# Kernel tuning notes

Hardware: AMD Instinct MI355X
Metric: run time of the kernel (lower is better)

Reference implementation:

```python
import jax, jax.numpy as jnp
import numpy as np
import math

D_MODEL = 1024
N_HEADS = 16
HEAD_DIM = D_MODEL // N_HEADS
N_LEVELS = 4
B = 8
MAX_LEN = 1024
LN_EPS = 1e-5


def setup_inputs() -> dict:
    key = jax.random.key(0)
    ks = jax.random.split(key, 6)
    lengths = np.array([1024, 768, 512, 896, 640, 1024, 576, 704], dtype=np.int32)
    N = int(lengths.sum())  # 6144
    batch_offsets = jnp.asarray(np.concatenate([[0], np.cumsum(lengths)]).astype(np.int32))
    x = jax.random.normal(ks[0], (N, D_MODEL), jnp.float32)
    levels = jax.random.randint(ks[1], (N, 1), 0, N_LEVELS).astype(jnp.float32)
    coords = jax.random.uniform(ks[2], (N, 2), jnp.float32) * 64.0
    positions = jnp.concatenate([levels, coords], axis=-1)  # [N, 3] = (level, y, x)
    ln_gamma = jnp.ones((D_MODEL,), jnp.float32)
    ln_beta = jnp.zeros((D_MODEL,), jnp.float32)
    w_qkv = jax.random.normal(ks[3], (D_MODEL, 3 * D_MODEL), jnp.float32) / math.sqrt(D_MODEL)
    w_out = jax.random.normal(ks[4], (D_MODEL, D_MODEL), jnp.float32) / math.sqrt(D_MODEL)
    # learned per-level, per-head rotary frequencies for 2 spatial coords
    base = 10.0 ** (-2.0 * np.arange(HEAD_DIM // 2) / HEAD_DIM)  # rope_theta = 10.0
    rope_freqs = (jnp.asarray(base, jnp.float32)[None, None, :, None]
                  * (1.0 + 0.1 * jax.random.normal(ks[5], (N_LEVELS, N_HEADS, HEAD_DIM // 2, 2), jnp.float32)))
    return {"x": x, "positions": positions, "batch_offsets": batch_offsets,
            "ln_gamma": ln_gamma, "ln_beta": ln_beta, "w_qkv": w_qkv,
            "w_out": w_out, "rope_freqs": rope_freqs}


def _layernorm(x, g, b):
    mu = jnp.mean(x, axis=-1, keepdims=True)
    var = jnp.mean(jnp.square(x - mu), axis=-1, keepdims=True)
    return (x - mu) * jax.lax.rsqrt(var + LN_EPS) * g + b


def _forward(x, positions, batch_offsets, ln_gamma, ln_beta, w_qkv, w_out, rope_freqs):
    N = x.shape[0]
    residual = x
    h = _layernorm(x, ln_gamma, ln_beta)
    q, k, v = jnp.split(h @ w_qkv, 3, axis=-1)  # each [N, D]

    # ragged -> padded batch layout
    tok = jnp.arange(N)
    batch_ids = jnp.searchsorted(batch_offsets[1:], tok, side='right')  # [N]
    pos_in_seq = tok - batch_offsets[batch_ids]                         # [N]
    lengths = batch_offsets[1:] - batch_offsets[:-1]                    # [B]
    valid = jnp.arange(MAX_LEN)[None, :] < lengths[:, None]             # [B, L]

    def pad(t, fill=0.0):
        out = jnp.full((B, MAX_LEN) + t.shape[1:], fill, t.dtype)
        return out.at[batch_ids, pos_in_seq].set(t)

    qp = pad(q).reshape(B, MAX_LEN, N_HEADS, HEAD_DIM)
    kp = pad(k).reshape(B, MAX_LEN, N_HEADS, HEAD_DIM)
    vp = pad(v).reshape(B, MAX_LEN, N_HEADS, HEAD_DIM)
    posp = pad(positions, fill=1.0)  # padded positions filled with ones (as in torch code)

    # multilevel RoPE: per-level learned freqs over 2 spatial coords
    lvl = jnp.clip(posp[..., 0].astype(jnp.int32), 0, N_LEVELS - 1)  # [B, L]
    f = rope_freqs[lvl]                                              # [B, L, H, K, 2]
    ang = jnp.einsum('blhkc,blc->blhk', f, posp[..., 1:])            # [B, L, H, K]
    cos, sin = jnp.cos(ang), jnp.sin(ang)

    def rot(t):  # rotate consecutive pairs of head_dim
        t = t.reshape(B, MAX_LEN, N_HEADS, HEAD_DIM // 2, 2)
        a, b = t[..., 0], t[..., 1]
        return jnp.stack([a * cos - b * sin, a * sin + b * cos], axis=-1).reshape(
            B, MAX_LEN, N_HEADS, HEAD_DIM)

    qr, kr = rot(qp), rot(kp)

    # masked SDPA (padded keys excluded; padded query rows are dropped on un-pad)
    scale = 1.0 / math.sqrt(HEAD_DIM)
    scores = jnp.einsum('blhd,bmhd->bhlm', qr, kr) * scale
    scores = jnp.where(valid[:, None, None, :], scores, jnp.float32(-1e9))
    attn = jax.nn.softmax(scores, axis=-1)
    o = jnp.einsum('bhlm,bmhd->blhd', attn, vp).reshape(B, MAX_LEN, D_MODEL)

    o = o[batch_ids, pos_in_seq]  # back to packed [N, D]
    return o @ w_out + residual


def reference(x, positions, batch_offsets, ln_gamma, ln_beta, w_qkv, w_out, rope_freqs):
    return _forward(x, positions, batch_offsets, ln_gamma, ln_beta, w_qkv, w_out, rope_freqs)
```

## Files before the change

### kernel.cpp

```cpp
#include <hip/hip_runtime.h>


typedef float  f32x4  __attribute__((ext_vector_type(4)));
typedef __bf16 bf16x8 __attribute__((ext_vector_type(8)));
typedef __bf16 bf16x4 __attribute__((ext_vector_type(4)));
typedef short  s16x4  __attribute__((ext_vector_type(4)));
typedef short  s16x8  __attribute__((ext_vector_type(8)));
typedef unsigned short u16x4 __attribute__((ext_vector_type(4)));

typedef __attribute__((address_space(1))) void as1_void_t;
typedef __attribute__((address_space(3))) void as3_void_t;

static __device__ __forceinline__ unsigned short f2bf(float f) {
  unsigned int u = __float_as_uint(f);
  u += 0x7fffu + ((u >> 16) & 1u);
  return (unsigned short)(u >> 16);
}
static __device__ __forceinline__ float bf2f(unsigned short s) {
  return __uint_as_float(((unsigned int)s) << 16);
}

static __device__ __forceinline__ void gload_lds16(const void* g, void* l) {
  __builtin_amdgcn_global_load_lds((as1_void_t*)g, (as3_void_t*)l, 16, 0, 0);
}

static __device__ __forceinline__ f32x4 mfma32(bf16x8 a, bf16x8 b, f32x4 c) {
  return __builtin_amdgcn_mfma_f32_16x16x32_bf16(a, b, c, 0, 0, 0);
}
static __device__ __forceinline__ f32x4 mfma16(s16x4 a, s16x4 b, f32x4 c) {
  return __builtin_amdgcn_mfma_f32_16x16x16bf16_1k(a, b, c, 0, 0, 0);
}

__global__ __launch_bounds__(256) void ln_kernel(
    const float* __restrict__ x, const float* __restrict__ gamma,
    const float* __restrict__ beta, unsigned short* __restrict__ h, int Ntok) {
  int row  = blockIdx.x * 4 + (threadIdx.x >> 6);
  int lane = threadIdx.x & 63;
  const float* xr = x + (size_t)row * 1024;
  f32x4 v[4];
  float s = 0.f, ss = 0.f;
#pragma unroll
  for (int c = 0; c < 4; ++c) {
    v[c] = *(const f32x4*)(xr + c * 256 + lane * 4);
#pragma unroll
    for (int j = 0; j < 4; ++j) { s += v[c][j]; ss += v[c][j] * v[c][j]; }
  }
#pragma unroll
  for (int d = 1; d < 64; d <<= 1) {
    s  += __shfl_xor(s, d);
    ss += __shfl_xor(ss, d);
  }
  float mu  = s * (1.f / 1024.f);
  float var = ss * (1.f / 1024.f) - mu * mu;
  float inv = rsqrtf(var + 1e-5f);
#pragma unroll
  for (int c = 0; c < 4; ++c) {
    f32x4 gv = *(const f32x4*)(gamma + c * 256 + lane * 4);
    f32x4 bv = *(const f32x4*)(beta  + c * 256 + lane * 4);
    u16x4 hv;
#pragma unroll
    for (int j = 0; j < 4; ++j) hv[j] = f2bf((v[c][j] - mu) * inv * gv[j] + bv[j]);
    *(u16x4*)(h + (size_t)row * 1024 + c * 256 + lane * 4) = hv;
  }
}

__global__ __launch_bounds__(256) void transpose_bf16(
    const float* __restrict__ in, unsigned short* __restrict__ out, int R, int C) {
  __shared__ unsigned short tile[64][65];
  int c0 = blockIdx.x * 64, r0 = blockIdx.y * 64;
  int t = threadIdx.x;
  int tr = t >> 6, tc = t & 63;
#pragma unroll
  for (int i = 0; i < 16; ++i) {
    int rr = i * 4 + tr;
    tile[tc][rr] = f2bf(in[(size_t)(r0 + rr) * C + c0 + tc]);
  }
  __syncthreads();
#pragma unroll
  for (int i = 0; i < 16; ++i) {
    int cc = i * 4 + tr;
    out[(size_t)(c0 + cc) * R + r0 + tc] = tile[cc][tc];
  }
}

template <int MODE>
__global__ __launch_bounds__(256) void gemm_bt(
    const unsigned short* __restrict__ A, const unsigned short* __restrict__ Bt,
    const float* __restrict__ residual, float* __restrict__ Cf,
    unsigned short* __restrict__ Cqkv, int M, int Ncols, int K) {
  __shared__ unsigned short Alds[128 * 32];
  __shared__ unsigned short Blds[128 * 32];
  int n0 = blockIdx.x * 128, m0 = blockIdx.y * 128;
  int t = threadIdx.x, lane = t & 63, wave = t >> 6;
  int wr = wave >> 1, wc = wave & 1;
  int r = lane & 15, g = lane >> 4;
  f32x4 acc[4][4] = {};

  int srow = lane >> 2;
  int scol = (lane & 3) * 8;

  for (int k0 = 0; k0 < K; k0 += 32) {
    __syncthreads();
#pragma unroll
    for (int c = 0; c < 2; ++c) {
      int seg = wave * 2 + c;
      gload_lds16(A  + (size_t)(m0 + seg * 16 + srow) * K + k0 + scol,
                  Alds + seg * 16 * 32);
      gload_lds16(Bt + (size_t)(n0 + seg * 16 + srow) * K + k0 + scol,
                  Blds + seg * 16 * 32);
    }
    __syncthreads();
    bf16x8 a[4], b[4];
#pragma unroll
    for (int m = 0; m < 4; ++m)
      a[m] = *(const bf16x8*)(Alds + (wr * 64 + m * 16 + r) * 32 + g * 8);
#pragma unroll
    for (int n = 0; n < 4; ++n)
      b[n] = *(const bf16x8*)(Blds + (wc * 64 + n * 16 + r) * 32 + g * 8);
#pragma unroll
    for (int m = 0; m < 4; ++m)
#pragma unroll
      for (int n = 0; n < 4; ++n)
        acc[m][n] = mfma32(a[m], b[n], acc[m][n]);
  }

#pragma unroll
  for (int mi = 0; mi < 4; ++mi) {
    int grow0 = m0 + wr * 64 + mi * 16 + g * 4;
#pragma unroll
    for (int ni = 0; ni < 4; ++ni) {
      int gcol = n0 + wc * 64 + ni * 16 + r;
      f32x4 v = acc[mi][ni];
#pragma unroll
      for (int e = 0; e < 4; ++e) {
        int grow = grow0 + e;
        if (MODE == 0) {
          Cf[(size_t)grow * Ncols + gcol] =
              v[e] + residual[(size_t)grow * Ncols + gcol];
        } else {
          int which = gcol >> 10, rem = gcol & 1023, hh = rem >> 6, d = rem & 63;
          Cqkv[((size_t)(which * 16 + hh) * M + grow) * 64 + d] = f2bf(v[e]);
        }
      }
    }
  }
}

__global__ __launch_bounds__(256) void rope_kernel(
    unsigned short* __restrict__ QKV, const float* __restrict__ pos,
    const float* __restrict__ freqs, int Ntok) {
  int t = blockIdx.x * 256 + threadIdx.x;
  if (t >= Ntok * 512) return;
  int kk = t & 31, h = (t >> 5) & 15, i = t >> 9;
  float lvlf = pos[i * 3 + 0];
  float py   = pos[i * 3 + 1];
  float px   = pos[i * 3 + 2];
  int lvl = (int)lvlf;
  lvl = lvl < 0 ? 0 : (lvl > 3 ? 3 : lvl);
  const float* fp = freqs + (((lvl * 16 + h) * 32 + kk) << 1);
  float ang = fp[0] * py + fp[1] * px;
  float s, c;
  __sincosf(ang, &s, &c);
  size_t qoff = ((size_t)h * Ntok + i) * 64 + 2 * kk;
  size_t koff = qoff + (size_t)16 * Ntok * 64;
  unsigned int q2 = *(const unsigned int*)(QKV + qoff);
  float qa = bf2f((unsigned short)(q2 & 0xffff));
  float qb = bf2f((unsigned short)(q2 >> 16));
  *(unsigned int*)(QKV + qoff) =
      (unsigned int)f2bf(qa * c - qb * s) | ((unsigned int)f2bf(qa * s + qb * c) << 16);
  unsigned int k2 = *(const unsigned int*)(QKV + koff);
  float ka = bf2f((unsigned short)(k2 & 0xffff));
  float kb = bf2f((unsigned short)(k2 >> 16));
  *(unsigned int*)(QKV + koff) =
      (unsigned int)f2bf(ka * c - kb * s) | ((unsigned int)f2bf(ka * s + kb * c) << 16);
}

__global__ __launch_bounds__(256) void vtrans_kernel(
    const unsigned short* __restrict__ Vp, unsigned short* __restrict__ VtG,
    int Ntok) {
  __shared__ unsigned short tile[64][72];
  int blk = blockIdx.x;
  int h = blk & 15, t0 = (blk >> 4) * 64;
  int t = threadIdx.x;
  {
    int tok = t >> 2, dc = (t & 3) * 16;
    const unsigned short* src = Vp + ((size_t)h * Ntok + t0 + tok) * 64 + dc;
    *(s16x8*)&tile[tok][dc]     = *(const s16x8*)src;
    *(s16x8*)&tile[tok][dc + 8] = *(const s16x8*)(src + 8);
  }
  __syncthreads();
  {
    int d = t >> 2, tc = (t & 3) * 16;
    s16x8 o0, o1;
#pragma unroll
    for (int j = 0; j < 8; ++j) {
      o0[j] = (short)tile[tc + j][d];
      o1[j] = (short)tile[tc + 8 + j][d];
    }
    unsigned short* dst = VtG + (size_t)(h * 64 + d) * Ntok + t0 + tc;
    *(s16x8*)dst       = o0;
    *(s16x8*)(dst + 8) = o1;
  }
}

__global__ __launch_bounds__(128, 3) void attn_kernel(
    const unsigned short* __restrict__ QKV,
    const unsigned short* __restrict__ VtG, const int* __restrict__ boff,
    unsigned short* __restrict__ O, int Ntok) {
  __shared__ unsigned short Klds[64][72];
  __shared__ unsigned short Vt[64][72];
  const float SCALE_LOG2 = 0.125f * 1.44269504088896340736f;
  const s16x4 ones16 = {(short)0x3F80, (short)0x3F80, (short)0x3F80, (short)0x3F80};

  int bid = blockIdx.x;
  int x = bid & 7, i = bid >> 3;
  int qblk = i & 15;
  int p = x + 8 * (i >> 4);
  int h = p & 15, b = p >> 4;
  int off = boff[b], len = boff[b + 1] - off;
  int q0 = qblk * 64;
  if (q0 >= len) return;
  int t = threadIdx.x, lane = t & 63, wave = t >> 6;
  int r = lane & 15, g = lane >> 4;
  const unsigned short* Qg = QKV + (size_t)h * Ntok * 64;
  const unsigned short* Kg = QKV + (size_t)(16 + h) * Ntok * 64;
  int qmax = off + len - 1;

  bf16x8 qf[2][2];
#pragma unroll
  for (int qi = 0; qi < 2; ++qi) {
    int qtok = off + q0 + wave * 32 + qi * 16 + r;
    if (qtok > qmax) qtok = qmax;
#pragma unroll
    for (int c = 0; c < 2; ++c)
      qf[qi][c] = *(const bf16x8*)(Qg + (size_t)qtok * 64 + c * 32 + g * 8);
  }

  float m[2] = {-1e30f, -1e30f};
  f32x4 o[2][4] = {};
  f32x4 o_sum[2] = {};

  int srow = t >> 1, sseg = t & 1;
  const unsigned short* Vrow = VtG + (size_t)(h * 64 + srow) * Ntok;

  s16x8 kr[4], vr[4];
  {
    int ktok = off + srow; if (ktok > qmax) ktok = qmax;
#pragma unroll
    for (int c = 0; c < 4; ++c)
      kr[c] = *(const s16x8*)(Kg + (size_t)ktok * 64 + sseg * 32 + c * 8);
#pragma unroll
    for (int c = 0; c < 4; ++c) {
      int tc = sseg * 32 + c * 8; if (tc + 8 > len) tc = len - 8;
      vr[c] = *(const s16x8*)(Vrow + off + tc);
    }
  }

  for (int kt = 0; kt < len; kt += 64) {
    asm volatile("s_waitcnt lgkmcnt(0)" ::: "memory");
    __builtin_amdgcn_s_barrier();
    __builtin_amdgcn_sched_barrier(0);
#pragma unroll
    for (int c = 0; c < 4; ++c) {
      *(s16x8*)&Klds[srow][sseg * 32 + c * 8] = kr[c];
      *(s16x8*)&Vt[srow][sseg * 32 + c * 8]   = vr[c];
    }
    int ktn = kt + 64;
    if (ktn < len) {
      int ktok = off + ktn + srow; if (ktok > qmax) ktok = qmax;
#pragma unroll
      for (int c = 0; c < 4; ++c)
        kr[c] = *(const s16x8*)(Kg + (size_t)ktok * 64 + sseg * 32 + c * 8);
#pragma unroll
      for (int c = 0; c < 4; ++c) {
        int tc = ktn + sseg * 32 + c * 8; if (tc + 8 > len) tc = len - 8;
        vr[c] = *(const s16x8*)(Vrow + off + tc);
      }
    }
    asm volatile("s_waitcnt lgkmcnt(0)" ::: "memory");
    __builtin_amdgcn_s_barrier();
    __builtin_amdgcn_sched_barrier(0);

    f32x4 s[2][4];
    __builtin_amdgcn_s_setprio(1);
#pragma unroll
    for (int sub = 0; sub < 4; ++sub) {
      bf16x8 ka0 = *(const bf16x8*)(&Klds[sub * 16 + r][g * 8]);
      bf16x8 ka1 = *(const bf16x8*)(&Klds[sub * 16 + r][32 + g * 8]);
#pragma unroll
      for (int qi = 0; qi < 2; ++qi) {
        f32x4 acc = {};
        acc = mfma32(ka0, qf[qi][0], acc);
        acc = mfma32(ka1, qf[qi][1], acc);
        s[qi][sub] = acc;
      }
    }
    __builtin_amdgcn_s_setprio(0);

    bool tail = (kt + 64 > len);
    s16x4 pf[2][4];
#pragma unroll
    for (int qi = 0; qi < 2; ++qi) {
      float sc[4][4];
      float ms[4];
#pragma unroll
      for (int sub = 0; sub < 4; ++sub) {
#pragma unroll
        for (int e = 0; e < 4; ++e) {
          float v = s[qi][sub][e];
          if (tail && (kt + sub * 16 + 4 * g + e >= len)) v = -1e30f;
          sc[sub][e] = v;
        }
        ms[sub] = fmaxf(fmaxf(sc[sub][0], sc[sub][1]),
                        fmaxf(sc[sub][2], sc[sub][3]));
      }
      float tmax = fmaxf(fmaxf(ms[0], ms[1]), fmaxf(ms[2], ms[3]));
      float mq = m[qi];
      if (!__all(tmax * SCALE_LOG2 <= mq + 8.f)) {
        float tm = tmax * SCALE_LOG2;
        tm = fmaxf(tm, __shfl_xor(tm, 16));
        tm = fmaxf(tm, __shfl_xor(tm, 32));
        float mnew = fmaxf(mq, tm);
        float alpha = exp2f(mq - mnew);
        m[qi] = mnew; mq = mnew;
#pragma unroll
        for (int e = 0; e < 4; ++e) o_sum[qi][e] *= alpha;
#pragma unroll
        for (int dt = 0; dt < 4; ++dt)
#pragma unroll
          for (int e = 0; e < 4; ++e) o[qi][dt][e] *= alpha;
      }
#pragma unroll
      for (int sub = 0; sub < 4; ++sub) {
        bf16x4 pb;
#pragma unroll
        for (int e = 0; e < 4; ++e)
          pb[e] = (__bf16)exp2f(fmaf(sc[sub][e], SCALE_LOG2, -mq));
        pf[qi][sub] = __builtin_bit_cast(s16x4, pb);
      }
    }

    __builtin_amdgcn_s_setprio(1);
#pragma unroll
    for (int sub = 0; sub < 4; ++sub) {
      o_sum[0] = mfma16(pf[0][sub], ones16, o_sum[0]);
      o_sum[1] = mfma16(pf[1][sub], ones16, o_sum[1]);
    }
#pragma unroll
    for (int dt = 0; dt < 4; ++dt)
#pragma unroll
      for (int sub = 0; sub < 4; ++sub) {
        s16x4 vf = *(const s16x4*)(&Vt[dt * 16 + r][sub * 16 + 4 * g]);
#pragma unroll
        for (int qi = 0; qi < 2; ++qi)
          o[qi][dt] = mfma16(pf[qi][sub], vf, o[qi][dt]);
      }
    __builtin_amdgcn_s_setprio(0);
  }

#pragma unroll
  for (int qi = 0; qi < 2; ++qi) {
    float il[4];
#pragma unroll
    for (int e = 0; e < 4; ++e) il[e] = 1.0f / o_sum[qi][e];
#pragma unroll
    for (int dt = 0; dt < 4; ++dt)
#pragma unroll
      for (int e = 0; e < 4; ++e) {
        int tl = q0 + wave * 32 + qi * 16 + 4 * g + e;
        if (tl < len)
          O[(size_t)(off + tl) * 1024 + h * 64 + dt * 16 + r] =
              f2bf(o[qi][dt][e] * il[e]);
      }
  }
}

extern "C" void kernel_launch(void* const* d_in, const int* in_sizes, int n_in,
                              void* d_out, int out_size, void* d_ws, size_t ws_size,
                              hipStream_t stream) {
  const float* x     = (const float*)d_in[0];
  const float* pos   = (const float*)d_in[1];
  const int*   boff  = (const int*)d_in[2];
  const float* gamma = (const float*)d_in[3];
  const float* beta  = (const float*)d_in[4];
  const float* wqkv  = (const float*)d_in[5];
  const float* wout  = (const float*)d_in[6];
  const float* freqs = (const float*)d_in[7];
  float* out = (float*)d_out;
  int N  = in_sizes[0] / 1024;
  int Bn = in_sizes[2] - 1;

  char* ws = (char*)d_ws;
  unsigned short* wqkvT = (unsigned short*)ws;
  unsigned short* woutT = (unsigned short*)(ws + (size_t)3072 * 1024 * 2);
  unsigned short* QKV   = (unsigned short*)(ws + (size_t)3072 * 1024 * 2 +
                                            (size_t)1024 * 1024 * 2);
  size_t qkvBytes = (size_t)48 * N * 64 * 2;
  unsigned short* hbuf = (unsigned short*)((char*)QKV + qkvBytes);
  unsigned short* VtG  = hbuf;
  unsigned short* Vp   = QKV + (size_t)32 * N * 64;
  unsigned short* Obuf = Vp;

  ln_kernel<<<N / 4, 256, 0, stream>>>(x, gamma, beta, hbuf, N);
  transpose_bf16<<<dim3(3072 / 64, 1024 / 64), 256, 0, stream>>>(wqkv, wqkvT, 1024, 3072);
  transpose_bf16<<<dim3(1024 / 64, 1024 / 64), 256, 0, stream>>>(wout, woutT, 1024, 1024);
  gemm_bt<1><<<dim3(3072 / 128, N / 128), 256, 0, stream>>>(
      hbuf, wqkvT, nullptr, nullptr, QKV, N, 3072, 1024);
  rope_kernel<<<(N * 512) / 256, 256, 0, stream>>>(QKV, pos, freqs, N);
  vtrans_kernel<<<16 * (N / 64), 256, 0, stream>>>(Vp, VtG, N);
  attn_kernel<<<Bn * 16 * 16, 128, 0, stream>>>(QKV, VtG, boff, Obuf, N);
  gemm_bt<0><<<dim3(1024 / 128, N / 128), 256, 0, stream>>>(
      Obuf, woutT, x, out, nullptr, N, 1024, 1024);
}
```

Before: 191.3 us.

## Use compact ragged attention grid and narrower output-projection tiles

```diff
diff --git a/kernel.cpp b/kernel.cpp
--- a/kernel.cpp
+++ b/kernel.cpp
@@ -83,11 +83,9 @@
   }
 }
 
-template <int MODE>
-__global__ __launch_bounds__(256) void gemm_bt(
+__global__ __launch_bounds__(256) void gemm_qkv(
     const unsigned short* __restrict__ A, const unsigned short* __restrict__ Bt,
-    const float* __restrict__ residual, float* __restrict__ Cf,
-    unsigned short* __restrict__ Cqkv, int M, int Ncols, int K) {
+    unsigned short* __restrict__ Cqkv, int M, int K) {
   __shared__ unsigned short Alds[128 * 32];
   __shared__ unsigned short Blds[128 * 32];
   int n0 = blockIdx.x * 128, m0 = blockIdx.y * 128;
@@ -133,15 +131,64 @@
       f32x4 v = acc[mi][ni];
 #pragma unroll
       for (int e = 0; e < 4; ++e) {
-        int grow = grow0 + e;
-        if (MODE == 0) {
-          Cf[(size_t)grow * Ncols + gcol] =
-              v[e] + residual[(size_t)grow * Ncols + gcol];
-        } else {
-          int which = gcol >> 10, rem = gcol & 1023, hh = rem >> 6, d = rem & 63;
-          Cqkv[((size_t)(which * 16 + hh) * M + grow) * 64 + d] = f2bf(v[e]);
-        }
-      }
+        int which = gcol >> 10, rem = gcol & 1023, hh = rem >> 6, d = rem & 63;
+        Cqkv[((size_t)(which * 16 + hh) * M + grow0 + e) * 64 + d] = f2bf(v[e]);
+      }
+    }
+  }
+}
+
+__global__ __launch_bounds__(256) void gemm_n64(
+    const unsigned short* __restrict__ A, const unsigned short* __restrict__ Bt,
+    const float* __restrict__ residual, float* __restrict__ Cf,
+    int M, int Ncols, int K) {
+  __shared__ unsigned short Alds[128 * 32];
+  __shared__ unsigned short Blds[64 * 32];
+  int n0 = blockIdx.x * 64, m0 = blockIdx.y * 128;
+  int t = threadIdx.x, lane = t & 63, wave = t >> 6;
+  int wr = wave >> 1, wc = wave & 1;
+  int r = lane & 15, g = lane >> 4;
+  f32x4 acc[4][2] = {};
+
+  int srow = lane >> 2;
+  int scol = (lane & 3) * 8;
+
+  for (int k0 = 0; k0 < K; k0 += 32) {
+    __syncthreads();
+#pragma unroll
+    for (int c = 0; c < 2; ++c) {
+      int seg = wave * 2 + c;
+      gload_lds16(A + (size_t)(m0 + seg * 16 + srow) * K + k0 + scol,
+                  Alds + seg * 16 * 32);
+    }
+    gload_lds16(Bt + (size_t)(n0 + wave * 16 + srow) * K + k0 + scol,
+                Blds + wave * 16 * 32);
+    __syncthreads();
+    bf16x8 a[4], b[2];
+#pragma unroll
+    for (int m = 0; m < 4; ++m)
+      a[m] = *(const bf16x8*)(Alds + (wr * 64 + m * 16 + r) * 32 + g * 8);
+#pragma unroll
+    for (int n = 0; n < 2; ++n)
+      b[n] = *(const bf16x8*)(Blds + (wc * 32 + n * 16 + r) * 32 + g * 8);
+#pragma unroll
+    for (int m = 0; m < 4; ++m)
+#pragma unroll
+      for (int n = 0; n < 2; ++n)
+        acc[m][n] = mfma32(a[m], b[n], acc[m][n]);
+  }
+
+#pragma unroll
+  for (int mi = 0; mi < 4; ++mi) {
+    int grow0 = m0 + wr * 64 + mi * 16 + g * 4;
+#pragma unroll
+    for (int ni = 0; ni < 2; ++ni) {
+      int gcol = n0 + wc * 32 + ni * 16 + r;
+      f32x4 v = acc[mi][ni];
+#pragma unroll
+      for (int e = 0; e < 4; ++e)
+        Cf[(size_t)(grow0 + e) * Ncols + gcol] =
+            v[e] + residual[(size_t)(grow0 + e) * Ncols + gcol];
     }
   }
 }
@@ -206,22 +253,28 @@
 __global__ __launch_bounds__(128, 3) void attn_kernel(
     const unsigned short* __restrict__ QKV,
     const unsigned short* __restrict__ VtG, const int* __restrict__ boff,
-    unsigned short* __restrict__ O, int Ntok) {
+    unsigned short* __restrict__ O, int Ntok, int Bn) {
   __shared__ unsigned short Klds[64][72];
   __shared__ unsigned short Vt[64][72];
   const float SCALE_LOG2 = 0.125f * 1.44269504088896340736f;
   const s16x4 ones16 = {(short)0x3F80, (short)0x3F80, (short)0x3F80, (short)0x3F80};
 
   int bid = blockIdx.x;
-  int x = bid & 7, i = bid >> 3;
-  int qblk = i & 15;
-  int p = x + 8 * (i >> 4);
-  int h = p & 15, b = p >> 4;
+  int nqb = Ntok >> 6;
+  int qpx = nqb >> 3;
+  int x = bid & 7, k = bid >> 3;
+  int g = (k % qpx) * 8 + x;
+  int h = k / qpx;
+  int gt = g << 6;
+  int b = 0;
+#pragma unroll
+  for (int j = 1; j < 8; ++j)
+    if (j < Bn && boff[j] <= gt) b = j;
   int off = boff[b], len = boff[b + 1] - off;
-  int q0 = qblk * 64;
-  if (q0 >= len) return;
+  int q0 = gt - off;
+
   int t = threadIdx.x, lane = t & 63, wave = t >> 6;
-  int r = lane & 15, g = lane >> 4;
+  int r = lane & 15, g4 = lane >> 4;
   const unsigned short* Qg = QKV + (size_t)h * Ntok * 64;
   const unsigned short* Kg = QKV + (size_t)(16 + h) * Ntok * 64;
   int qmax = off + len - 1;
@@ -233,7 +286,7 @@
     if (qtok > qmax) qtok = qmax;
 #pragma unroll
     for (int c = 0; c < 2; ++c)
-      qf[qi][c] = *(const bf16x8*)(Qg + (size_t)qtok * 64 + c * 32 + g * 8);
+      qf[qi][c] = *(const bf16x8*)(Qg + (size_t)qtok * 64 + c * 32 + g4 * 8);
   }
 
   float m[2] = {-1e30f, -1e30f};
@@ -285,8 +338,8 @@
     __builtin_amdgcn_s_setprio(1);
 #pragma unroll
     for (int sub = 0; sub < 4; ++sub) {
-      bf16x8 ka0 = *(const bf16x8*)(&Klds[sub * 16 + r][g * 8]);
-      bf16x8 ka1 = *(const bf16x8*)(&Klds[sub * 16 + r][32 + g * 8]);
+      bf16x8 ka0 = *(const bf16x8*)(&Klds[sub * 16 + r][g4 * 8]);
+      bf16x8 ka1 = *(const bf16x8*)(&Klds[sub * 16 + r][32 + g4 * 8]);
 #pragma unroll
       for (int qi = 0; qi < 2; ++qi) {
         f32x4 acc = {};
@@ -308,7 +361,7 @@
 #pragma unroll
         for (int e = 0; e < 4; ++e) {
           float v = s[qi][sub][e];
-          if (tail && (kt + sub * 16 + 4 * g + e >= len)) v = -1e30f;
+          if (tail && (kt + sub * 16 + 4 * g4 + e >= len)) v = -1e30f;
           sc[sub][e] = v;
         }
         ms[sub] = fmaxf(fmaxf(sc[sub][0], sc[sub][1]),
@@ -350,7 +403,7 @@
     for (int dt = 0; dt < 4; ++dt)
 #pragma unroll
       for (int sub = 0; sub < 4; ++sub) {
-        s16x4 vf = *(const s16x4*)(&Vt[dt * 16 + r][sub * 16 + 4 * g]);
+        s16x4 vf = *(const s16x4*)(&Vt[dt * 16 + r][sub * 16 + 4 * g4]);
 #pragma unroll
         for (int qi = 0; qi < 2; ++qi)
           o[qi][dt] = mfma16(pf[qi][sub], vf, o[qi][dt]);
@@ -367,7 +420,7 @@
     for (int dt = 0; dt < 4; ++dt)
 #pragma unroll
       for (int e = 0; e < 4; ++e) {
-        int tl = q0 + wave * 32 + qi * 16 + 4 * g + e;
+        int tl = q0 + wave * 32 + qi * 16 + 4 * g4 + e;
         if (tl < len)
           O[(size_t)(off + tl) * 1024 + h * 64 + dt * 16 + r] =
               f2bf(o[qi][dt][e] * il[e]);
@@ -404,11 +457,11 @@
   ln_kernel<<<N / 4, 256, 0, stream>>>(x, gamma, beta, hbuf, N);
   transpose_bf16<<<dim3(3072 / 64, 1024 / 64), 256, 0, stream>>>(wqkv, wqkvT, 1024, 3072);
   transpose_bf16<<<dim3(1024 / 64, 1024 / 64), 256, 0, stream>>>(wout, woutT, 1024, 1024);
-  gemm_bt<1><<<dim3(3072 / 128, N / 128), 256, 0, stream>>>(
-      hbuf, wqkvT, nullptr, nullptr, QKV, N, 3072, 1024);
+  gemm_qkv<<<dim3(3072 / 128, N / 128), 256, 0, stream>>>(
+      hbuf, wqkvT, QKV, N, 1024);
   rope_kernel<<<(N * 512) / 256, 256, 0, stream>>>(QKV, pos, freqs, N);
   vtrans_kernel<<<16 * (N / 64), 256, 0, stream>>>(Vp, VtG, N);
-  attn_kernel<<<Bn * 16 * 16, 128, 0, stream>>>(QKV, VtG, boff, Obuf, N);
-  gemm_bt<0><<<dim3(1024 / 128, N / 128), 256, 0, stream>>>(
-      Obuf, woutT, x, out, nullptr, N, 1024, 1024);
-}
+  attn_kernel<<<16 * (N / 64), 128, 0, stream>>>(QKV, VtG, boff, Obuf, N, Bn);
+  gemm_n64<<<dim3(1024 / 64, N / 128), 256, 0, stream>>>(
+      Obuf, woutT, x, out, N, 1024, 1024);
+}
```

Measured after the change: 194.2 us. About the same (+1.5%).
